# Kernel tuning notes

Hardware: AMD Instinct MI355X
Metric: run time of the kernel (lower is better)

The kernel has to match this reference:

```python
import jax, jax.numpy as jnp
import numpy as np

EPSILON = 1e-8
B, T, H = 4, 4096, 2048          # batch, seq, hidden_dim
D, NH, K = 256, 4, 32            # belief_dim, num_heads, top_k
NB, NG = 65536, 16               # n_beliefs, n_goals
NEG_INF = -1e30


def setup_inputs() -> dict:
    key = jax.random.key(0)
    ks = jax.random.split(key, 8)
    hidden = jax.random.normal(ks[0], (B, T, H), dtype=jnp.float32)
    beliefs = jax.random.normal(ks[1], (NB, D), dtype=jnp.float32)
    active_mask = jax.random.bernoulli(ks[2], 0.5, (NB,))
    goal_embeddings = jax.random.normal(ks[3], (NG, D), dtype=jnp.float32)
    goal_priorities = jax.random.uniform(ks[4], (NG,), dtype=jnp.float32)
    # torch nn.Linear weights are [out_features, in_features]
    Wq = jax.random.normal(ks[5], (NH * D, H), dtype=jnp.float32) / np.float32(np.sqrt(H))
    Wo = jax.random.normal(ks[6], (H, NH * D), dtype=jnp.float32) / np.float32(np.sqrt(NH * D))
    log_temperature = jax.random.normal(ks[7], (NH,), dtype=jnp.float32) * 0.1
    return {"hidden": hidden, "beliefs": beliefs, "active_mask": active_mask,
            "goal_embeddings": goal_embeddings, "goal_priorities": goal_priorities,
            "Wq": Wq, "Wo": Wo, "log_temperature": log_temperature}


def reference(hidden, beliefs, active_mask, goal_embeddings, goal_priorities, Wq, Wo, log_temperature):
    # --- rough-score top-k pre-filter over active beliefs (N_active > top_k path) ---
    mean_query = hidden.mean(axis=(0, 1))                      # [H]
    rough_query = (Wq @ mean_query).reshape(NH, D).mean(axis=0)  # [D]
    radii = jnp.maximum(jnp.linalg.norm(beliefs, axis=-1), EPSILON)  # [NB]
    angles = beliefs / radii[:, None]                          # [NB, D]
    rough_scores = angles @ rough_query                        # [NB]
    # mask-gather: inactive beliefs get -inf so topk selects only active ones
    rough_scores = jnp.where(active_mask, rough_scores, NEG_INF)
    _, topk_idx = jax.lax.top_k(rough_scores, K)               # [K]
    active_beliefs = beliefs[topk_idx]                         # [K, D]

    # --- angle-normalized keys, raw values ---
    a_radii = jnp.maximum(jnp.linalg.norm(active_beliefs, axis=-1), EPSILON)
    keys = active_beliefs / a_radii[:, None]                   # [K, D]
    values = active_beliefs                                    # [K, D]

    # --- per-head queries and temperature ---
    queries = (hidden @ Wq.T).reshape(B, T, NH, D)             # [B,T,h,D]
    temperature = jnp.maximum(jnp.exp(log_temperature), 0.1)   # [h]
    scores = jnp.einsum('bthd,nd->bthn', queries, keys) / np.float32(np.sqrt(D))
    scores = scores * temperature[None, None, :, None]         # [B,T,h,K]

    # --- goal-similarity bias ---
    g_radii = jnp.maximum(jnp.linalg.norm(goal_embeddings, axis=-1), EPSILON)
    goal_angles = goal_embeddings / g_radii[:, None]           # [NG, D]
    sim = (keys @ goal_angles.T) * goal_priorities[None, :]    # [K, NG]
    goal_bias = sim.max(axis=-1)                               # [K], same for all heads
    scores = scores + goal_bias[None, None, None, :]

    attn = jax.nn.softmax(scores, axis=-1)                     # [B,T,h,K]
    retrieved = jnp.einsum('bthn,nd->bthd', attn, values).reshape(B, T, NH * D)
    return retrieved @ Wo.T                                    # [B,T,H]
```

## Files before the change

### kernel.cpp

```cpp
#include <hip/hip_runtime.h>

typedef unsigned int u32;
typedef unsigned short u16;
typedef unsigned long long u64;

typedef __bf16 bf16x8 __attribute__((ext_vector_type(8)));
typedef float f32x4 __attribute__((ext_vector_type(4)));

#define DEV __device__ __forceinline__

DEV u16 f2bf(float f) {
  u32 u = __float_as_uint(f);
  u += 0x7fffu + ((u >> 16) & 1u);
  return (u16)(u >> 16);
}
DEV float bf2f(u16 u) { return __uint_as_float((u32)u << 16); }

DEV void gld_lds16(const void* g, void* l) {
  __builtin_amdgcn_global_load_lds((const __attribute__((address_space(1))) u32*)g,
                                   (__attribute__((address_space(3))) u32*)l, 16, 0, 0);
}

DEV u64 packkey(float f, u32 idx) {
  u32 u = __float_as_uint(f);
  u = (u & 0x80000000u) ? ~u : (u | 0x80000000u);
  return ((u64)u << 32) | (u32)(~idx);
}

__global__ __launch_bounds__(256) void k_conv_mean(const float4* __restrict__ hidden4,
                                                   ushort4* __restrict__ hb4,
                                                   float4* __restrict__ partial4) {
  const int c4 = blockIdx.x * 256 + threadIdx.x;
  const int r0 = blockIdx.y * 64;
  float4 s = {0.f, 0.f, 0.f, 0.f};
  for (int r = 0; r < 64; r++) {
    float4 v = hidden4[(size_t)(r0 + r) * 512 + c4];
    ushort4 o; o.x = f2bf(v.x); o.y = f2bf(v.y); o.z = f2bf(v.z); o.w = f2bf(v.w);
    hb4[(size_t)(r0 + r) * 512 + c4] = o;
    s.x += v.x; s.y += v.y; s.z += v.z; s.w += v.w;
  }
  partial4[blockIdx.y * 512 + c4] = s;
}

__global__ __launch_bounds__(256) void k_mean(const float* __restrict__ partial,
                                              float* __restrict__ mean) {
  __shared__ float red[256];
  const int t = threadIdx.x;
  const int c = t & 15, s = t >> 4;
  const int col = blockIdx.x * 16 + c;
  float acc = 0.f;
  for (int ch = s; ch < 256; ch += 16) acc += partial[ch * 2048 + col];
  red[t] = acc;
  __syncthreads();
  for (int st = 8; st > 0; st >>= 1) {
    if (s < st) red[t] += red[t + st * 16];
    __syncthreads();
  }
  if (s == 0) mean[col] = red[c] * (1.0f / 16384.0f);
}

__global__ __launch_bounds__(256) void k_rq(const float* __restrict__ Wq,
                                            const float* __restrict__ mean,
                                            float* __restrict__ rq) {
  const int w = threadIdx.x >> 6, l = threadIdx.x & 63;
  const int row = blockIdx.x * 4 + w;
  float s = 0.f;
#pragma unroll
  for (int j = 0; j < 32; j++)
    s = fmaf(Wq[(size_t)row * 2048 + j * 64 + l], mean[j * 64 + l], s);
  for (int mk = 1; mk < 64; mk <<= 1) s += __shfl_xor(s, mk);
  if (l == 0) atomicAdd(&rq[row & 255], 0.25f * s);
}

__global__ __launch_bounds__(256) void k_rough(const float* __restrict__ beliefs,
                                               const void* __restrict__ amask,
                                               const float* __restrict__ rq,
                                               u64* __restrict__ keys) {
  const int t = threadIdx.x, w = t >> 6, l = t & 63;
  const int n = blockIdx.x * 4 + w;
  u32 mv = ((const u32*)amask)[l];
  bool isInt = (__ballot(mv > 1u) == 0ull);
  float4 b = *(const float4*)(beliefs + (size_t)n * 256 + l * 4);
  float4 qv = *(const float4*)(rq + l * 4);
  float dot = b.x * qv.x + b.y * qv.y + b.z * qv.z + b.w * qv.w;
  float ss = b.x * b.x + b.y * b.y + b.z * b.z + b.w * b.w;
  for (int mk = 1; mk < 64; mk <<= 1) { dot += __shfl_xor(dot, mk); ss += __shfl_xor(ss, mk); }
  if (l == 0) {
    bool act = isInt ? (((const int*)amask)[n] != 0)
                     : (((const unsigned char*)amask)[n] != 0);
    float score = act ? dot / fmaxf(sqrtf(ss), 1e-8f) : -1e30f;
    keys[n] = packkey(score, (u32)n);
  }
}

__global__ __launch_bounds__(256) void k_top1(const u64* __restrict__ keys,
                                              u64* __restrict__ cands) {
  __shared__ u64 ws[128];
  const int t = threadIdx.x, w = t >> 6, l = t & 63;
  const u64* src = keys + (size_t)blockIdx.x * 1024;
  u64 v0 = src[t], v1 = src[t + 256], v2 = src[t + 512], v3 = src[t + 768];
  for (int r = 0; r < 32; r++) {
    u64 a = v0 > v1 ? v0 : v1;
    u64 b = v2 > v3 ? v2 : v3;
    u64 m = a > b ? a : b;
#pragma unroll
    for (int mk = 1; mk < 64; mk <<= 1) { u64 o = __shfl_xor(m, mk); m = o > m ? o : m; }
    if (l == 0) ws[w * 32 + r] = m;
    v0 = (v0 == m) ? 0ull : v0;
    v1 = (v1 == m) ? 0ull : v1;
    v2 = (v2 == m) ? 0ull : v2;
    v3 = (v3 == m) ? 0ull : v3;
  }
  __syncthreads();
  if (w == 0) {
    u64 u0 = ws[l], u1 = ws[64 + l];
    for (int r = 0; r < 32; r++) {
      u64 m = u0 > u1 ? u0 : u1;
#pragma unroll
      for (int mk = 1; mk < 64; mk <<= 1) { u64 o = __shfl_xor(m, mk); m = o > m ? o : m; }
      if (l == 0) cands[blockIdx.x * 32 + r] = m;
      u0 = (u0 == m) ? 0ull : u0;
      u1 = (u1 == m) ? 0ull : u1;
    }
  }
}

__global__ __launch_bounds__(256) void k_top2_prep(const u64* __restrict__ cands,
                                                   const float* __restrict__ beliefs,
                                                   const float* __restrict__ goals,
                                                   const float* __restrict__ prio,
                                                   const float* __restrict__ logt,
                                                   float* __restrict__ keysf_g,
                                                   float* __restrict__ valsf_g,
                                                   float* __restrict__ biasO,
                                                   float* __restrict__ tempO) {
  __shared__ u64 ws[128];
  __shared__ int idxS[32];
  __shared__ float keysf[32 * 256];
  __shared__ float gradS[16];
  const int t = threadIdx.x, w = t >> 6, l = t & 63;
  u64 v[8];
#pragma unroll
  for (int i = 0; i < 8; i++) v[i] = cands[t + i * 256];
  for (int r = 0; r < 32; r++) {
    u64 m = v[0];
#pragma unroll
    for (int i = 1; i < 8; i++) m = v[i] > m ? v[i] : m;
#pragma unroll
    for (int mk = 1; mk < 64; mk <<= 1) { u64 o = __shfl_xor(m, mk); m = o > m ? o : m; }
    if (l == 0) ws[w * 32 + r] = m;
#pragma unroll
    for (int i = 0; i < 8; i++) v[i] = (v[i] == m) ? 0ull : v[i];
  }
  __syncthreads();
  if (w == 0) {
    u64 u0 = ws[l], u1 = ws[64 + l];
    for (int r = 0; r < 32; r++) {
      u64 m = u0 > u1 ? u0 : u1;
#pragma unroll
      for (int mk = 1; mk < 64; mk <<= 1) { u64 o = __shfl_xor(m, mk); m = o > m ? o : m; }
      if (l == 0) idxS[r] = (int)(~(u32)(m & 0xffffffffull));
      u0 = (u0 == m) ? 0ull : u0;
      u1 = (u1 == m) ? 0ull : u1;
    }
  }
  __syncthreads();
  for (int g = w * 4; g < w * 4 + 4; g++) {
    float4 gv = *(const float4*)(goals + g * 256 + l * 4);
    float ss = gv.x * gv.x + gv.y * gv.y + gv.z * gv.z + gv.w * gv.w;
    for (int mk = 1; mk < 64; mk <<= 1) ss += __shfl_xor(ss, mk);
    if (l == 0) gradS[g] = fmaxf(sqrtf(ss), 1e-8f);
  }
  for (int kk = w * 8; kk < w * 8 + 8; kk++) {
    int idx = idxS[kk];
    float4 bv = *(const float4*)(beliefs + (size_t)idx * 256 + l * 4);
    float ss = bv.x * bv.x + bv.y * bv.y + bv.z * bv.z + bv.w * bv.w;
    for (int mk = 1; mk < 64; mk <<= 1) ss += __shfl_xor(ss, mk);
    float rr = 1.0f / fmaxf(sqrtf(ss), 1e-8f);
    float4 kv; kv.x = bv.x * rr; kv.y = bv.y * rr; kv.z = bv.z * rr; kv.w = bv.w * rr;
    *(float4*)&keysf[kk * 256 + l * 4] = kv;
    *(float4*)&keysf_g[kk * 256 + l * 4] = kv;
    *(float4*)&valsf_g[kk * 256 + l * 4] = bv;
  }
  __syncthreads();
  for (int kk = w * 8; kk < w * 8 + 8; kk++) {
    float4 kv = *(const float4*)&keysf[kk * 256 + l * 4];
    float best = -1e30f;
    for (int g = 0; g < 16; g++) {
      float4 gv = *(const float4*)(goals + g * 256 + l * 4);
      float d = kv.x * gv.x + kv.y * gv.y + kv.z * gv.z + kv.w * gv.w;
      for (int mk = 1; mk < 64; mk <<= 1) d += __shfl_xor(d, mk);
      float sim = d / gradS[g] * prio[g];
      best = fmaxf(best, sim);
    }
    if (l == 0) biasO[kk] = best;
  }
  if (t < 4) tempO[t] = fmaxf(__expf(logt[t]), 0.1f);
}

__global__ __launch_bounds__(256) void k_build(const float* __restrict__ Wq,
                                               const float* __restrict__ Wo,
                                               const float* __restrict__ keysf_g,
                                               const float* __restrict__ valsf_g,
                                               u16* __restrict__ Kp,
                                               u16* __restrict__ VWoT) {
  __shared__ __align__(16) float sbuf[16384];
  const int t = threadIdx.x;
  if (blockIdx.x < 128) {
    float* keysS = sbuf;
    float* WqS = sbuf + 8192;
    const int h = blockIdx.x >> 5;
    const int c0 = (blockIdx.x & 31) * 64;
#pragma unroll
    for (int it = 0; it < 32; it++) keysS[t + it * 256] = keysf_g[t + it * 256];
    const int n0 = (t >> 5) * 4;
    const int c2 = (t & 31) * 2;
    float acc[4][2] = {};
    for (int dc = 0; dc < 4; dc++) {
      __syncthreads();
#pragma unroll
      for (int it = 0; it < 16; it++) {
        int i = t + it * 256;
        int r = i >> 6, c = i & 63;
        WqS[i] = Wq[(size_t)(h * 256 + dc * 64 + r) * 2048 + c0 + c];
      }
      __syncthreads();
      for (int d4 = 0; d4 < 16; d4++) {
        float4 kv[4];
#pragma unroll
        for (int i = 0; i < 4; i++)
          kv[i] = *(const float4*)&keysS[(n0 + i) * 256 + dc * 64 + d4 * 4];
#pragma unroll
        for (int dd = 0; dd < 4; dd++) {
          float2 w2 = *(const float2*)&WqS[(d4 * 4 + dd) * 64 + c2];
          float kvd[4] = {kv[0][dd], kv[1][dd], kv[2][dd], kv[3][dd]};
#pragma unroll
          for (int i = 0; i < 4; i++) {
            acc[i][0] = fmaf(kvd[i], w2.x, acc[i][0]);
            acc[i][1] = fmaf(kvd[i], w2.y, acc[i][1]);
          }
        }
      }
    }
#pragma unroll
    for (int i = 0; i < 4; i++) {
      u32 pk = (u32)f2bf(acc[i][0]) | ((u32)f2bf(acc[i][1]) << 16);
      *(u32*)&Kp[(size_t)(h * 32 + n0 + i) * 2048 + c0 + c2] = pk;
    }
  } else {
    float* valsS = sbuf;
    float* WoS = sbuf + 8192;
    const int c0 = (blockIdx.x - 128) * 32;
#pragma unroll
    for (int it = 0; it < 32; it++) valsS[t + it * 256] = valsf_g[t + it * 256];
    const int c = t >> 3;
    const int n0 = (t & 7) * 4;
    for (int h = 0; h < 4; h++) {
      __syncthreads();
#pragma unroll
      for (int it = 0; it < 32; it++) {
        int i = t + it * 256;
        int r = i >> 8, d = i & 255;
        WoS[i] = Wo[(size_t)(c0 + r) * 1024 + h * 256 + d];
      }
      __syncthreads();
      float acc[4] = {};
      for (int d4 = 0; d4 < 64; d4++) {
        float4 w4 = *(const float4*)&WoS[c * 256 + d4 * 4];
#pragma unroll
        for (int i = 0; i < 4; i++) {
          float4 kv = *(const float4*)&valsS[(n0 + i) * 256 + d4 * 4];
          acc[i] = fmaf(w4.x, kv.x, acc[i]);
          acc[i] = fmaf(w4.y, kv.y, acc[i]);
          acc[i] = fmaf(w4.z, kv.z, acc[i]);
          acc[i] = fmaf(w4.w, kv.w, acc[i]);
        }
      }
      ushort4 o; o.x = f2bf(acc[0]); o.y = f2bf(acc[1]); o.z = f2bf(acc[2]); o.w = f2bf(acc[3]);
      *(ushort4*)&VWoT[(size_t)(c0 + c) * 128 + h * 32 + n0] = o;
    }
  }
}

__global__ __launch_bounds__(512) void k_attn(const u16* __restrict__ hb,
                                              const u16* __restrict__ kp,
                                              const u16* __restrict__ vwot,
                                              const float* __restrict__ bias,
                                              const float* __restrict__ temp,
                                              float* __restrict__ out) {
  __shared__ __align__(16) u16 smem[57344];
  u16* Plds = smem + 49152;
  const int t = threadIdx.x;
  const int w = t >> 6, l = t & 63;
  const int q = l >> 4, c = l & 15;
  const int m0 = blockIdx.x * 64;
  const int rh = w >> 2, hd = w & 3;

  const float ts = temp[hd] * 0.0625f;
  const float b0 = bias[c], b1 = bias[16 + c];
  asm volatile("s_waitcnt vmcnt(0) lgkmcnt(0)" ::: "memory");

  const int rowA = t >> 3;
  const int cbA = (t & 7) ^ (rowA & 7);
  const u16* srcA = hb + (size_t)(m0 + rowA) * 2048 + cbA * 8;
  const int rowB1 = 64 + rowA;
  const int cbB0 = (t & 7) ^ (rowA & 7);
  const int cbB1 = (t & 7) ^ (rowB1 & 7);
  const u16* srcB0 = kp + (size_t)rowA * 2048 + cbB0 * 8;
  const u16* srcB1 = kp + (size_t)rowB1 * 2048 + cbB1 * 8;
  u16* dstA = smem + w * 512;
  u16* dstB0 = smem + 16384 + w * 512;
  u16* dstB1 = smem + 16384 + 4096 + w * 512;

  auto issue3 = [&](int j) {
    const int bo = j & 3;
    gld_lds16(srcA + j * 64, dstA + bo * 4096);
    gld_lds16(srcB0 + j * 64, dstB0 + bo * 8192);
    gld_lds16(srcB1 + j * 64, dstB1 + bo * 8192);
  };

  f32x4 acc[2][2] = {};
  issue3(0); issue3(1); issue3(2);

  for (int s = 0; s < 32; s++) {
    if (s <= 29)      asm volatile("s_waitcnt vmcnt(6)" ::: "memory");
    else if (s == 30) asm volatile("s_waitcnt vmcnt(3)" ::: "memory");
    else              asm volatile("s_waitcnt vmcnt(0)" ::: "memory");
    __builtin_amdgcn_s_barrier();
    __builtin_amdgcn_sched_barrier(0);
    if (s < 29) issue3(s + 3);

    const u16* Ab = smem + (s & 3) * 4096;
    const u16* Bb = smem + 16384 + (s & 3) * 8192;
    bf16x8 af[2][2], bfr[2][2];
#pragma unroll
    for (int mi = 0; mi < 2; mi++) {
      const int ra = rh * 32 + mi * 16 + c;
#pragma unroll
      for (int ks = 0; ks < 2; ks++)
        af[mi][ks] = __builtin_bit_cast(bf16x8,
            *(const uint4*)&Ab[ra * 64 + (((ks * 4 + q) ^ (ra & 7)) * 8)]);
    }
#pragma unroll
    for (int ni = 0; ni < 2; ni++) {
      const int rb = hd * 32 + ni * 16 + c;
#pragma unroll
      for (int ks = 0; ks < 2; ks++)
        bfr[ni][ks] = __builtin_bit_cast(bf16x8,
            *(const uint4*)&Bb[rb * 64 + (((ks * 4 + q) ^ (rb & 7)) * 8)]);
    }
    asm volatile("s_waitcnt lgkmcnt(0)" ::: "memory");
    __builtin_amdgcn_sched_barrier(0);
#pragma unroll
    for (int ks = 0; ks < 2; ks++)
#pragma unroll
      for (int mi = 0; mi < 2; mi++)
#pragma unroll
        for (int ni = 0; ni < 2; ni++)
          acc[mi][ni] = __builtin_amdgcn_mfma_f32_16x16x32_bf16(af[mi][ks], bfr[ni][ks],
                                                                acc[mi][ni], 0, 0, 0);
  }

#pragma unroll
  for (int mi = 0; mi < 2; mi++) {
#pragma unroll
    for (int r = 0; r < 4; r++) {
      float v0 = fmaf(acc[mi][0][r], ts, b0);
      float v1 = fmaf(acc[mi][1][r], ts, b1);
      float m = fmaxf(v0, v1);
#pragma unroll
      for (int mk = 1; mk <= 8; mk <<= 1) m = fmaxf(m, __shfl_xor(m, mk));
      float e0 = __expf(v0 - m), e1 = __expf(v1 - m);
      float sum = e0 + e1;
#pragma unroll
      for (int mk = 1; mk <= 8; mk <<= 1) sum += __shfl_xor(sum, mk);
      float inv = 1.0f / sum;
      const int rp = rh * 32 + mi * 16 + q * 4 + r;
      const int k0 = hd * 32 + c, k1 = k0 + 16;
      Plds[rp * 128 + (((k0 >> 3) ^ (rp & 7)) * 8) + (k0 & 7)] = f2bf(e0 * inv);
      Plds[rp * 128 + (((k1 >> 3) ^ (rp & 7)) * 8) + (k1 & 7)] = f2bf(e1 * inv);
    }
  }
  __syncthreads();

  const int rw = w & 3, chh = w >> 2;
  const int rp = rw * 16 + c;
  bf16x8 pa[4];
#pragma unroll
  for (int ks = 0; ks < 4; ks++)
    pa[ks] = __builtin_bit_cast(bf16x8,
        *(const uint4*)&Plds[rp * 128 + (((ks * 4 + q) ^ (rp & 7)) * 8)]);

  for (int cb = 0; cb < 32; cb++) {
    f32x4 oacc[2] = {};
#pragma unroll
    for (int ni = 0; ni < 2; ni++) {
      const int rv = cb * 64 + chh * 32 + ni * 16 + c;
      const u16* vr = vwot + (size_t)rv * 128 + q * 8;
#pragma unroll
      for (int ks = 0; ks < 4; ks++) {
        bf16x8 vb = __builtin_bit_cast(bf16x8, *(const uint4*)(vr + ks * 32));
        oacc[ni] = __builtin_amdgcn_mfma_f32_16x16x32_bf16(pa[ks], vb, oacc[ni], 0, 0, 0);
      }
    }
#pragma unroll
    for (int ni = 0; ni < 2; ni++) {
      const int col = cb * 64 + chh * 32 + ni * 16 + c;
#pragma unroll
      for (int r = 0; r < 4; r++)
        out[(size_t)(m0 + rw * 16 + q * 4 + r) * 2048 + col] = oacc[ni][r];
    }
  }
}

extern "C" void kernel_launch(void* const* d_in, const int* in_sizes, int n_in,
                              void* d_out, int out_size, void* d_ws, size_t ws_size,
                              hipStream_t stream) {
  const float* hidden = (const float*)d_in[0];
  const float* beliefs = (const float*)d_in[1];
  const void* amask = d_in[2];
  const float* goals = (const float*)d_in[3];
  const float* prio = (const float*)d_in[4];
  const float* Wq = (const float*)d_in[5];
  const float* Wo = (const float*)d_in[6];
  const float* logt = (const float*)d_in[7];
  float* out = (float*)d_out;

  char* ws = (char*)d_ws;
  size_t off = 0;
  auto alloc = [&](size_t bytes) { char* p = ws + off; off = (off + bytes + 255) & ~(size_t)255; return p; };
  u16* hb      = (u16*)alloc(67108864);
  u16* kp      = (u16*)alloc(524288);
  u16* vwot    = (u16*)alloc(524288);
  float* partial = (float*)alloc(2097152);
  float* meanq = (float*)alloc(8192);
  float* rq    = (float*)alloc(1024);
  u64* keys    = (u64*)alloc(524288);
  u64* cands   = (u64*)alloc(16384);
  float* keysf = (float*)alloc(32768);
  float* valsf = (float*)alloc(32768);
  float* biasv = (float*)alloc(128);
  float* tempv = (float*)alloc(16);

  hipMemsetAsync(rq, 0, 1024, stream);
  k_conv_mean<<<dim3(2, 256), 256, 0, stream>>>((const float4*)hidden, (ushort4*)hb, (float4*)partial);
  k_mean<<<128, 256, 0, stream>>>(partial, meanq);
  k_rq<<<256, 256, 0, stream>>>(Wq, meanq, rq);
  k_rough<<<16384, 256, 0, stream>>>(beliefs, amask, rq, keys);
  k_top1<<<64, 256, 0, stream>>>(keys, cands);
  k_top2_prep<<<1, 256, 0, stream>>>(cands, beliefs, goals, prio, logt, keysf, valsf, biasv, tempv);
  k_build<<<192, 256, 0, stream>>>(Wq, Wo, keysf, valsf, kp, vwot);
  k_attn<<<256, 512, 0, stream>>>(hb, kp, vwot, biasv, tempv, out);
}
```

Baseline: 527.8 us.

## Retile output GEMM so each wave covers all rows and reuses V-Wo fragments

The final P·(V·Wo) stage used to split the 64-row block into four 16-row strips, so each wave loaded its own V-Wo fragments for every column block. Now each wave keeps P fragments for all four row strips in registers and owns a contiguous 256-column range. Each loaded V-Wo fragment therefore feeds four MFMAs, which cuts global/L2 traffic for the fused weight. The cost is more VGPRs (16 P fragments plus 4 V fragments and 4 accumulators), which could lower occupancy, and the stores now go to a different column pattern.

```diff
diff --git a/kernel.cpp b/kernel.cpp
--- a/kernel.cpp
+++ b/kernel.cpp
@@ -383,33 +383,36 @@
   }
   __syncthreads();
 
-  const int rw = w & 3, chh = w >> 2;
-  const int rp = rw * 16 + c;
-  bf16x8 pa[4];
-#pragma unroll
-  for (int ks = 0; ks < 4; ks++)
-    pa[ks] = __builtin_bit_cast(bf16x8,
-        *(const uint4*)&Plds[rp * 128 + (((ks * 4 + q) ^ (rp & 7)) * 8)]);
-
-  for (int cb = 0; cb < 32; cb++) {
-    f32x4 oacc[2] = {};
-#pragma unroll
-    for (int ni = 0; ni < 2; ni++) {
-      const int rv = cb * 64 + chh * 32 + ni * 16 + c;
-      const u16* vr = vwot + (size_t)rv * 128 + q * 8;
-#pragma unroll
-      for (int ks = 0; ks < 4; ks++) {
-        bf16x8 vb = __builtin_bit_cast(bf16x8, *(const uint4*)(vr + ks * 32));
-        oacc[ni] = __builtin_amdgcn_mfma_f32_16x16x32_bf16(pa[ks], vb, oacc[ni], 0, 0, 0);
-      }
-    }
-#pragma unroll
-    for (int ni = 0; ni < 2; ni++) {
-      const int col = cb * 64 + chh * 32 + ni * 16 + c;
+  const int col0 = w * 256;
+  bf16x8 pa[4][4];
+#pragma unroll
+  for (int mi = 0; mi < 4; mi++) {
+    const int rp = mi * 16 + c;
+#pragma unroll
+    for (int ks = 0; ks < 4; ks++)
+      pa[mi][ks] = __builtin_bit_cast(bf16x8,
+          *(const uint4*)&Plds[rp * 128 + (((ks * 4 + q) ^ (rp & 7)) * 8)]);
+  }
+#pragma unroll
+  for (int ni = 0; ni < 16; ni++) {
+    const int rv = col0 + ni * 16 + c;
+    const u16* vr = vwot + (size_t)rv * 128 + q * 8;
+    bf16x8 vb[4];
+#pragma unroll
+    for (int ks = 0; ks < 4; ks++)
+      vb[ks] = __builtin_bit_cast(bf16x8, *(const uint4*)(vr + ks * 32));
+    f32x4 oacc[4] = {};
+#pragma unroll
+    for (int mi = 0; mi < 4; mi++)
+#pragma unroll
+      for (int ks = 0; ks < 4; ks++)
+        oacc[mi] = __builtin_amdgcn_mfma_f32_16x16x32_bf16(pa[mi][ks], vb[ks], oacc[mi], 0, 0, 0);
+    const int col = col0 + ni * 16 + c;
+#pragma unroll
+    for (int mi = 0; mi < 4; mi++)
 #pragma unroll
       for (int r = 0; r < 4; r++)
-        out[(size_t)(m0 + rw * 16 + q * 4 + r) * 2048 + col] = oacc[ni][r];
-    }
+        out[(size_t)(m0 + mi * 16 + q * 4 + r) * 2048 + col] = oacc[mi][r];
   }
 }
 
```

Result: faster. 505.2 us (-4.3%).
